# Performance work log

Measured on AMD Instinct MI355X. Metric: run time of the kernel, lower is better.

## Reference

```python
import jax, jax.numpy as jnp
import numpy as np

N_NODES = 100000
N_EDGES = 1600000
IN_F = 256
OUT_F = 64
ALPHA = 0.2  # LeakyReLU negative slope


def setup_inputs() -> dict:
    key = jax.random.key(0)
    k1, k2, k3, k4 = jax.random.split(key, 4)
    x = jax.random.normal(k1, (N_NODES, IN_F), dtype=jnp.float32)
    indices = jax.random.randint(k2, (2, N_EDGES), 0, N_NODES, dtype=jnp.int64)
    # xavier_uniform with gain=1.414 ~ U(-b, b), b = gain*sqrt(6/(fan_in+fan_out))
    bW = 1.414 * np.sqrt(6.0 / (IN_F + OUT_F))
    W = jax.random.uniform(k3, (IN_F, OUT_F), dtype=jnp.float32, minval=-bW, maxval=bW)
    ba = 1.414 * np.sqrt(6.0 / (2 * OUT_F + 1))
    a = jax.random.uniform(k4, (2 * OUT_F, 1), dtype=jnp.float32, minval=-ba, maxval=ba)
    return {"x": x, "indices": indices, "W": W, "a": a}


def reference(x, indices, W, a):
    # h = X @ W  -> [N, F_out]
    h = x @ W
    N = h.shape[0]
    src = indices[0]  # segment ids (softmax rows / aggregation targets)
    dst = indices[1]  # gathered neighbor features

    # e_ij = leakyrelu([h_i || h_j] @ a) = leakyrelu(h_i@a1 + h_j@a2)
    # (identical math to concatenation, avoids materializing [E, 2F])
    a1 = a[:OUT_F, 0]
    a2 = a[OUT_F:, 0]
    s1 = h @ a1  # [N]
    s2 = h @ a2  # [N]
    logits = s1[src] + s2[dst]  # [E]
    e = jnp.where(logits > 0, logits, ALPHA * logits)

    # segment softmax over edges grouped by src (sp_softmax)
    m = jax.ops.segment_max(e, src, num_segments=N)
    ex = jnp.exp(e - m[src])
    denom = jax.ops.segment_sum(ex, src, num_segments=N)
    att = ex / denom[src]  # [E]

    # h_prime[i] = sum_j att_ij * h_j  (sp_matmul: weighted scatter-aggregate)
    h_prime = jax.ops.segment_sum(att[:, None] * h[dst], src, num_segments=N)

    # concat=True -> ELU
    return jax.nn.elu(h_prime)
```

## Files before the change

kernel.cpp:

```cpp
#include <hip/hip_runtime.h>
#include <hip/hip_bf16.h>
#include <math.h>

#define NN 100000
#define NE 1600000
#define INF_ 256
#define OF 64

#define NPB 256
#define NB  ((NN + NPB - 1) / NPB)
#define P1B 256
#define CH  ((NE + P1B - 1) / P1B)
#define CAP 5120

constexpr float LRELU_ALPHA = 0.2f;

typedef __attribute__((ext_vector_type(8))) short short8;
typedef __attribute__((ext_vector_type(4))) float f32x4;

static __device__ __forceinline__ unsigned short f2bf(float f) {
    union { float f; unsigned int u; } v; v.f = f;
    unsigned int r = v.u + 0x7fff + ((v.u >> 16) & 1);
    return (unsigned short)(r >> 16);
}
static __device__ __forceinline__ float bf2f(unsigned short b) {
    union { unsigned int u; float f; } v; v.u = ((unsigned int)b) << 16;
    return v.f;
}
static __device__ __forceinline__ unsigned int pkbf(float a, float b) {
    union { __hip_bfloat162 h; unsigned int u; } c;
    c.h = __float22bfloat162_rn(make_float2(a, b));
    return c.u;
}

union S8 { short8 s; unsigned int u[4]; };

__global__ __launch_bounds__(256) void k_prep(const float* __restrict__ W,
                                              const float* __restrict__ a,
                                              float* __restrict__ wa) {
    int r = threadIdx.x;
    float t1 = 0.f, t2 = 0.f;
#pragma unroll 8
    for (int c = 0; c < OF; ++c) {
        float w = W[r * OF + c];
        t1 += w * a[c];
        t2 += w * a[OF + c];
    }
    wa[r] = t1;
    wa[256 + r] = t2;
}

__global__ __launch_bounds__(256) void k_gemm_mfma(const float* __restrict__ x,
                                                   const float* __restrict__ W,
                                                   const float* __restrict__ wa,
                                                   unsigned short* __restrict__ h,
                                                   float* __restrict__ s1,
                                                   float* __restrict__ s2) {
    __shared__ short Wf[2560 * 8];
    int tid = threadIdx.x;
    for (int i = tid; i < 2560; i += 256) {
        int ks = i / 320;
        int rem = i - ks * 320;
        int ct = rem >> 6;
        int l  = rem & 63;
        int kb = ks * 32 + ((l >> 4) << 3);
        int c  = l & 15;
        S8 v;
        if (ct < 4) {
            int col = ct * 16 + c;
#pragma unroll
            for (int j = 0; j < 4; ++j)
                v.u[j] = pkbf(W[(size_t)(kb + 2 * j) * OF + col],
                              W[(size_t)(kb + 2 * j + 1) * OF + col]);
        } else if (c < 2) {
            const float* src = wa + c * 256;
#pragma unroll
            for (int j = 0; j < 4; ++j)
                v.u[j] = pkbf(src[kb + 2 * j], src[kb + 2 * j + 1]);
        } else {
#pragma unroll
            for (int j = 0; j < 4; ++j) v.u[j] = 0u;
        }
        ((short8*)Wf)[i] = v.s;
    }
    __syncthreads();

    int wid = tid >> 6, lane = tid & 63;
    int rowbase = blockIdx.x * 128 + wid * 32;
    int r0 = rowbase + (lane & 15);
    int koff = (lane >> 4) << 3;

    f32x4 acc[2][5];
#pragma unroll
    for (int rt = 0; rt < 2; ++rt)
#pragma unroll
        for (int ct = 0; ct < 5; ++ct) acc[rt][ct] = (f32x4){0.f, 0.f, 0.f, 0.f};

#pragma unroll 1
    for (int ks = 0; ks < 8; ++ks) {
        S8 af[2];
#pragma unroll
        for (int rt = 0; rt < 2; ++rt) {
            int r = r0 + rt * 16;
            if (r < NN) {
                const float* p = x + (size_t)r * INF_ + ks * 32 + koff;
                float4 xa = *(const float4*)p;
                float4 xb = *(const float4*)(p + 4);
                af[rt].u[0] = pkbf(xa.x, xa.y);
                af[rt].u[1] = pkbf(xa.z, xa.w);
                af[rt].u[2] = pkbf(xb.x, xb.y);
                af[rt].u[3] = pkbf(xb.z, xb.w);
            } else {
#pragma unroll
                for (int j = 0; j < 4; ++j) af[rt].u[j] = 0u;
            }
        }
#pragma unroll
        for (int rt = 0; rt < 2; ++rt)
#pragma unroll
            for (int ct = 0; ct < 5; ++ct)
                acc[rt][ct] = __builtin_amdgcn_mfma_f32_16x16x32_bf16(
                    af[rt].s, ((short8*)Wf)[(ks * 5 + ct) * 64 + lane], acc[rt][ct], 0, 0, 0);
    }

    int c = lane & 15, rowq = lane >> 4;
#pragma unroll
    for (int rt = 0; rt < 2; ++rt) {
#pragma unroll
        for (int reg = 0; reg < 4; ++reg) {
            int r = rowbase + rt * 16 + rowq * 4 + reg;
            if (r < NN) {
#pragma unroll
                for (int ct = 0; ct < 4; ++ct)
                    h[(size_t)r * OF + ct * 16 + c] = f2bf(acc[rt][ct][reg]);
                float sv = acc[rt][4][reg];
                if (c == 0)      s1[r] = sv;
                else if (c == 1) s2[r] = sv;
            }
        }
    }
}

__global__ __launch_bounds__(256) void k_bhist(const int* __restrict__ idx,
                                               int* __restrict__ bcnt,
                                               int* __restrict__ blkhist) {
    __shared__ int hist[NB];
    int tid = threadIdx.x, blk = blockIdx.x;
    for (int i = tid; i < NB; i += 256) hist[i] = 0;
    __syncthreads();
    int e0 = blk * CH, e1 = min(e0 + CH, NE);
    for (int e = e0 + tid; e < e1; e += 256)
        atomicAdd(&hist[idx[e] >> 8], 1);
    __syncthreads();
    for (int b = tid; b < NB; b += 256) {
        int c = hist[b];
        blkhist[blk * NB + b] = c;
        if (c) atomicAdd(&bcnt[b], c);
    }
}

__global__ __launch_bounds__(512) void k_bscan(const int* __restrict__ bcnt,
                                               int* __restrict__ bbase,
                                               int* __restrict__ cur_b,
                                               int* __restrict__ start) {
    __shared__ int sc[512];
    int t = threadIdx.x;
    int v = (t < NB) ? bcnt[t] : 0;
    sc[t] = v; __syncthreads();
    for (int off = 1; off < 512; off <<= 1) {
        int x = (t >= off) ? sc[t - off] : 0;
        __syncthreads();
        sc[t] += x;
        __syncthreads();
    }
    if (t < NB) { int ex = sc[t] - v; bbase[t] = ex; cur_b[t] = ex; }
    if (t == 0) start[NN] = NE;
}

__global__ __launch_bounds__(256) void k_part1(const int* __restrict__ idx,
                                               const int* __restrict__ blkhist,
                                               int* __restrict__ cur_b,
                                               int2* __restrict__ pairs) {
    __shared__ int gbase[NB];
    __shared__ int lcur[NB];
    int tid = threadIdx.x, blk = blockIdx.x;
    for (int b = tid; b < NB; b += 256) {
        int c = blkhist[blk * NB + b];
        gbase[b] = c ? atomicAdd(&cur_b[b], c) : 0;
        lcur[b] = 0;
    }
    __syncthreads();
    int e0 = blk * CH, e1 = min(e0 + CH, NE);
    for (int e = e0 + tid; e < e1; e += 256) {
        int s = idx[e], d = idx[NE + e];
        int b = s >> 8;
        int p = atomicAdd(&lcur[b], 1);
        pairs[gbase[b] + p] = make_int2(s, d);
    }
}

__global__ __launch_bounds__(256) void k_part2(const int2* __restrict__ pairs,
                                               const int* __restrict__ bcnt,
                                               const int* __restrict__ bbase,
                                               int* __restrict__ start,
                                               int* __restrict__ sorted_dst) {
    __shared__ int2 stage[CAP];
    __shared__ int cnt[NPB];
    __shared__ int sc[NPB];
    int tid = threadIdx.x, b = blockIdx.x;
    int n = bcnt[b], gb = bbase[b];
    int node0 = b << 8;
    cnt[tid] = 0;
    __syncthreads();
    for (int i = tid; i < n; i += 256) {
        int2 pr = pairs[gb + i];
        if (i < CAP) stage[i] = pr;
        atomicAdd(&cnt[pr.x & (NPB - 1)], 1);
    }
    __syncthreads();
    int v = cnt[tid];
    sc[tid] = v; __syncthreads();
    for (int off = 1; off < NPB; off <<= 1) {
        int x = (tid >= off) ? sc[tid - off] : 0;
        __syncthreads();
        sc[tid] += x;
        __syncthreads();
    }
    int ex = sc[tid] - v;
    int g = node0 + tid;
    if (g < NN) start[g] = gb + ex;
    cnt[tid] = ex;
    __syncthreads();
    for (int i = tid; i < n; i += 256) {
        int2 pr = (i < CAP) ? stage[i] : pairs[gb + i];
        int p = atomicAdd(&cnt[pr.x & (NPB - 1)], 1);
        sorted_dst[gb + p] = pr.y;
    }
}

__global__ __launch_bounds__(256) void k_agg(const int* __restrict__ sorted_dst,
                                             const int* __restrict__ start,
                                             const float* __restrict__ s1,
                                             const float* __restrict__ s2,
                                             const unsigned short* __restrict__ h,
                                             float* __restrict__ out) {
    __shared__ int2 tile[4][64];
    int tid = threadIdx.x;
    int wid = tid >> 6, lane = tid & 63;
    int node = blockIdx.x * 4 + wid;
    if (node >= NN) return;

    int st = start[node];
    int dg = start[node + 1] - st;
    float s1n = s1[node];
    float den = 0.f, acc = 0.f;

    for (int base = 0; base < dg; base += 64) {
        int cnt = min(64, dg - base);
        int dj = 0; float exj = 0.f;
        if (lane < cnt) {
            dj = sorted_dst[st + base + lane];
            float lg = s1n + s2[dj];
            float el = lg > 0.f ? lg : LRELU_ALPHA * lg;
            exj = expf(el);
        }
        tile[wid][lane] = make_int2(dj, __float_as_int(exj));
        asm volatile("s_waitcnt lgkmcnt(0)" ::: "memory");
#pragma unroll 4
        for (int j = 0; j < cnt; ++j) {
            int2 pr = tile[wid][j];
            float e = __int_as_float(pr.y);
            den += e;
            acc += e * bf2f(h[(size_t)pr.x * OF + lane]);
        }
        asm volatile("" ::: "memory");
    }

    float inv = den > 0.f ? 1.f / den : 0.f;
    float v = acc * inv;
    out[(size_t)node * OF + lane] = v > 0.f ? v : expf(v) - 1.f;
}

extern "C" void kernel_launch(void* const* d_in, const int* in_sizes, int n_in,
                              void* d_out, int out_size, void* d_ws, size_t ws_size,
                              hipStream_t stream) {
    const float* x   = (const float*)d_in[0];
    const int*   idx = (const int*)d_in[1];
    const float* W   = (const float*)d_in[2];
    const float* a   = (const float*)d_in[3];
    float* out = (float*)d_out;

    char* ws = (char*)d_ws;
    unsigned short* h = (unsigned short*)ws;  ws += sizeof(unsigned short) * (size_t)NN * OF;
    int2* pairs       = (int2*)ws;            ws += sizeof(int2) * (size_t)NE;
    int*  sorted_dst  = (int*)ws;             ws += sizeof(int) * (size_t)NE;
    float* s1         = (float*)ws;           ws += sizeof(float) * NN;
    float* s2         = (float*)ws;           ws += sizeof(float) * NN;
    int*   start      = (int*)ws;             ws += sizeof(int) * (NN + 1);
    int*   bcnt       = (int*)ws;             ws += sizeof(int) * NB;
    int*   bbase      = (int*)ws;             ws += sizeof(int) * NB;
    int*   cur_b      = (int*)ws;             ws += sizeof(int) * NB;
    int*   blkhist    = (int*)ws;             ws += sizeof(int) * P1B * NB;
    float* wa         = (float*)ws;           ws += sizeof(float) * 512;

    hipMemsetAsync(bcnt, 0, sizeof(int) * NB, stream);
    k_prep<<<1, 256, 0, stream>>>(W, a, wa);
    k_gemm_mfma<<<(NN + 127) / 128, 256, 0, stream>>>(x, W, wa, h, s1, s2);
    k_bhist<<<P1B, 256, 0, stream>>>(idx, bcnt, blkhist);
    k_bscan<<<1, 512, 0, stream>>>(bcnt, bbase, cur_b, start);
    k_part1<<<P1B, 256, 0, stream>>>(idx, blkhist, cur_b, pairs);
    k_part2<<<NB, 256, 0, stream>>>(pairs, bcnt, bbase, start, sorted_dst);
    k_agg<<<(NN + 3) / 4, 256, 0, stream>>>(sorted_dst, start, s1, s2, h, out);
}
```

Baseline: 304.0 us.

## Replace global-scan CSR build with fixed-capacity bucket partition and overflow list

Result: faster. 295.2 us (-2.9%).

```diff
diff --git a/kernel.cpp b/kernel.cpp
--- a/kernel.cpp
+++ b/kernel.cpp
@@ -7,11 +7,12 @@
 #define INF_ 256
 #define OF 64
 
-#define NPB 256
-#define NB  ((NN + NPB - 1) / NPB)
-#define P1B 256
-#define CH  ((NE + P1B - 1) / P1B)
-#define CAP 5120
+#define NPB 128
+#define NB  782
+#define CAPB 2560
+#define P1B 512
+#define CH1 ((NE + P1B - 1) / P1B)
+#define OVCAP 8192
 
 constexpr float LRELU_ALPHA = 0.2f;
 
@@ -141,105 +142,99 @@
     }
 }
 
-__global__ __launch_bounds__(256) void k_bhist(const int* __restrict__ idx,
-                                               int* __restrict__ bcnt,
-                                               int* __restrict__ blkhist) {
+__global__ __launch_bounds__(256) void k_part1(const int* __restrict__ idx,
+                                               int* __restrict__ cur_b,
+                                               int* __restrict__ pairs,
+                                               int2* __restrict__ ov_list) {
     __shared__ int hist[NB];
+    __shared__ int gbase[NB];
     int tid = threadIdx.x, blk = blockIdx.x;
     for (int i = tid; i < NB; i += 256) hist[i] = 0;
     __syncthreads();
-    int e0 = blk * CH, e1 = min(e0 + CH, NE);
+    int e0 = blk * CH1, e1 = min(e0 + CH1, NE);
     for (int e = e0 + tid; e < e1; e += 256)
-        atomicAdd(&hist[idx[e] >> 8], 1);
-    __syncthreads();
-    for (int b = tid; b < NB; b += 256) {
-        int c = hist[b];
-        blkhist[blk * NB + b] = c;
-        if (c) atomicAdd(&bcnt[b], c);
-    }
-}
-
-__global__ __launch_bounds__(512) void k_bscan(const int* __restrict__ bcnt,
-                                               int* __restrict__ bbase,
-                                               int* __restrict__ cur_b,
-                                               int* __restrict__ start) {
-    __shared__ int sc[512];
-    int t = threadIdx.x;
-    int v = (t < NB) ? bcnt[t] : 0;
-    sc[t] = v; __syncthreads();
-    for (int off = 1; off < 512; off <<= 1) {
-        int x = (t >= off) ? sc[t - off] : 0;
-        __syncthreads();
-        sc[t] += x;
-        __syncthreads();
-    }
-    if (t < NB) { int ex = sc[t] - v; bbase[t] = ex; cur_b[t] = ex; }
-    if (t == 0) start[NN] = NE;
-}
-
-__global__ __launch_bounds__(256) void k_part1(const int* __restrict__ idx,
-                                               const int* __restrict__ blkhist,
-                                               int* __restrict__ cur_b,
-                                               int2* __restrict__ pairs) {
-    __shared__ int gbase[NB];
-    __shared__ int lcur[NB];
-    int tid = threadIdx.x, blk = blockIdx.x;
-    for (int b = tid; b < NB; b += 256) {
-        int c = blkhist[blk * NB + b];
-        gbase[b] = c ? atomicAdd(&cur_b[b], c) : 0;
-        lcur[b] = 0;
-    }
-    __syncthreads();
-    int e0 = blk * CH, e1 = min(e0 + CH, NE);
+        atomicAdd(&hist[idx[e] >> 7], 1);
+    __syncthreads();
+    for (int i = tid; i < NB; i += 256) {
+        int c = hist[i];
+        gbase[i] = c ? atomicAdd(&cur_b[i], c) : 0;
+        hist[i] = 0;
+    }
+    __syncthreads();
     for (int e = e0 + tid; e < e1; e += 256) {
         int s = idx[e], d = idx[NE + e];
-        int b = s >> 8;
-        int p = atomicAdd(&lcur[b], 1);
-        pairs[gbase[b] + p] = make_int2(s, d);
-    }
-}
-
-__global__ __launch_bounds__(256) void k_part2(const int2* __restrict__ pairs,
-                                               const int* __restrict__ bcnt,
-                                               const int* __restrict__ bbase,
+        int b = s >> 7;
+        int p = gbase[b] + atomicAdd(&hist[b], 1);
+        if (p < CAPB) pairs[b * CAPB + p] = ((s & 127) << 17) | d;
+        else {
+            int j = atomicAdd(&cur_b[NB], 1);
+            if (j < OVCAP) ov_list[j] = make_int2(s, d);
+        }
+    }
+}
+
+__global__ __launch_bounds__(256) void k_part2(const int* __restrict__ pairs,
+                                               const int* __restrict__ cur_b,
+                                               const int2* __restrict__ ov_list,
                                                int* __restrict__ start,
+                                               int* __restrict__ deg,
                                                int* __restrict__ sorted_dst) {
-    __shared__ int2 stage[CAP];
-    __shared__ int cnt[NPB];
-    __shared__ int sc[NPB];
+    __shared__ int stage[CAPB + 128];
+    __shared__ int cnt[NPB], pfx[NPB];
+    __shared__ int extra;
     int tid = threadIdx.x, b = blockIdx.x;
-    int n = bcnt[b], gb = bbase[b];
-    int node0 = b << 8;
-    cnt[tid] = 0;
-    __syncthreads();
-    for (int i = tid; i < n; i += 256) {
-        int2 pr = pairs[gb + i];
-        if (i < CAP) stage[i] = pr;
-        atomicAdd(&cnt[pr.x & (NPB - 1)], 1);
-    }
-    __syncthreads();
-    int v = cnt[tid];
-    sc[tid] = v; __syncthreads();
+    if (tid < NPB) cnt[tid] = 0;
+    if (tid == 0) extra = 0;
+    __syncthreads();
+
+    int t_b = cur_b[b];
+    int nin = min(t_b, CAPB);
+    for (int i = tid; i < nin; i += 256) {
+        int v = pairs[b * CAPB + i];
+        stage[i] = v;
+        atomicAdd(&cnt[v >> 17], 1);
+    }
+    if (t_b > CAPB) {
+        int ovn = min(cur_b[NB], OVCAP);
+        for (int i = tid; i < ovn; i += 256) {
+            int2 e = ov_list[i];
+            if ((e.x >> 7) == b) {
+                int k = atomicAdd(&extra, 1);
+                if (k < 128) {
+                    stage[CAPB + k] = ((e.x & 127) << 17) | e.y;
+                    atomicAdd(&cnt[e.x & 127], 1);
+                }
+            }
+        }
+    }
+    __syncthreads();
+    int ntot = nin + min(extra, 128);
+
+    if (tid < NPB) pfx[tid] = cnt[tid];
+    __syncthreads();
     for (int off = 1; off < NPB; off <<= 1) {
-        int x = (tid >= off) ? sc[tid - off] : 0;
+        int xv = (tid >= off && tid < NPB) ? pfx[tid - off] : 0;
         __syncthreads();
-        sc[tid] += x;
+        if (tid < NPB) pfx[tid] += xv;
         __syncthreads();
     }
-    int ex = sc[tid] - v;
-    int g = node0 + tid;
-    if (g < NN) start[g] = gb + ex;
-    cnt[tid] = ex;
-    __syncthreads();
-    for (int i = tid; i < n; i += 256) {
-        int2 pr = (i < CAP) ? stage[i] : pairs[gb + i];
-        int p = atomicAdd(&cnt[pr.x & (NPB - 1)], 1);
-        sorted_dst[gb + p] = pr.y;
+    if (tid < NPB) {
+        int ex = pfx[tid] - cnt[tid];
+        int g = b * NPB + tid;
+        if (g < NN) { start[g] = b * CAPB + ex; deg[g] = cnt[tid]; }
+        cnt[tid] = ex;
+    }
+    __syncthreads();
+    for (int i = tid; i < ntot; i += 256) {
+        int v = stage[i];
+        int p = atomicAdd(&cnt[v >> 17], 1);
+        sorted_dst[b * CAPB + p] = v & 0x1FFFF;
     }
 }
 
 __global__ __launch_bounds__(256) void k_agg(const int* __restrict__ sorted_dst,
                                              const int* __restrict__ start,
+                                             const int* __restrict__ deg,
                                              const float* __restrict__ s1,
                                              const float* __restrict__ s2,
                                              const unsigned short* __restrict__ h,
@@ -251,7 +246,7 @@
     if (node >= NN) return;
 
     int st = start[node];
-    int dg = start[node + 1] - st;
+    int dg = deg[node];
     float s1n = s1[node];
     float den = 0.f, acc = 0.f;
 
@@ -292,23 +287,20 @@
 
     char* ws = (char*)d_ws;
     unsigned short* h = (unsigned short*)ws;  ws += sizeof(unsigned short) * (size_t)NN * OF;
-    int2* pairs       = (int2*)ws;            ws += sizeof(int2) * (size_t)NE;
-    int*  sorted_dst  = (int*)ws;             ws += sizeof(int) * (size_t)NE;
+    int*  pairs       = (int*)ws;             ws += sizeof(int) * (size_t)NB * CAPB;
+    int*  sorted_dst  = (int*)ws;             ws += sizeof(int) * (size_t)NB * CAPB;
     float* s1         = (float*)ws;           ws += sizeof(float) * NN;
     float* s2         = (float*)ws;           ws += sizeof(float) * NN;
-    int*   start      = (int*)ws;             ws += sizeof(int) * (NN + 1);
-    int*   bcnt       = (int*)ws;             ws += sizeof(int) * NB;
-    int*   bbase      = (int*)ws;             ws += sizeof(int) * NB;
-    int*   cur_b      = (int*)ws;             ws += sizeof(int) * NB;
-    int*   blkhist    = (int*)ws;             ws += sizeof(int) * P1B * NB;
+    int*   start      = (int*)ws;             ws += sizeof(int) * NN;
+    int*   deg        = (int*)ws;             ws += sizeof(int) * NN;
+    int*   cur_b      = (int*)ws;             ws += sizeof(int) * (NB + 16);
+    int2*  ov_list    = (int2*)ws;            ws += sizeof(int2) * OVCAP;
     float* wa         = (float*)ws;           ws += sizeof(float) * 512;
 
-    hipMemsetAsync(bcnt, 0, sizeof(int) * NB, stream);
+    hipMemsetAsync(cur_b, 0, sizeof(int) * (NB + 16), stream);
     k_prep<<<1, 256, 0, stream>>>(W, a, wa);
     k_gemm_mfma<<<(NN + 127) / 128, 256, 0, stream>>>(x, W, wa, h, s1, s2);
-    k_bhist<<<P1B, 256, 0, stream>>>(idx, bcnt, blkhist);
-    k_bscan<<<1, 512, 0, stream>>>(bcnt, bbase, cur_b, start);
-    k_part1<<<P1B, 256, 0, stream>>>(idx, blkhist, cur_b, pairs);
-    k_part2<<<NB, 256, 0, stream>>>(pairs, bcnt, bbase, start, sorted_dst);
-    k_agg<<<(NN + 3) / 4, 256, 0, stream>>>(sorted_dst, start, s1, s2, h, out);
-}
+    k_part1<<<P1B, 256, 0, stream>>>(idx, cur_b, pairs, ov_list);
+    k_part2<<<NB, 256, 0, stream>>>(pairs, cur_b, ov_list, start, deg, sorted_dst);
+    k_agg<<<(NN + 3) / 4, 256, 0, stream>>>(sorted_dst, start, deg, s1, s2, h, out);
+}
```
